# Kernel tuning notes

Hardware: AMD Instinct MI355X
Metric: run time of the kernel (lower is better)

Reference implementation:

```python
import math
import jax, jax.numpy as jnp
import numpy as np

H, D_H = 16, 128  # heads, head_dim; d = H*D_H = 2048

def _heads_view(w, rank):
    # w: (d, r) -> (H, r, d_h), matching torch view(H, d_h, r).transpose(1, 2)
    return jnp.transpose(w.reshape(H, D_H, rank), (0, 2, 1))

def setup_inputs() -> dict:
    key = jax.random.key(0)
    ks = jax.random.split(key, 9)
    d, rq, rk, rv = 2048, 512, 512, 512
    B, T = 2, 2048
    s = 0.02  # GPT-2 style init scale keeps logits numerically sane
    return {
        "x": jax.random.normal(ks[0], (B, T, d), dtype=jnp.float32),
        "q_down_w": jax.random.normal(ks[1], (rq, d), dtype=jnp.float32) * s,
        "k_down_w": jax.random.normal(ks[2], (rk, d), dtype=jnp.float32) * s,
        "v_down_w": jax.random.normal(ks[3], (rv, d), dtype=jnp.float32) * s,
        "q_up_w": jax.random.normal(ks[4], (d, rq), dtype=jnp.float32) * s,
        "k_up_w": jax.random.normal(ks[5], (d, rk), dtype=jnp.float32) * s,
        "v_up_w": jax.random.normal(ks[6], (d, rv), dtype=jnp.float32) * s,
        "out_w": jax.random.normal(ks[7], (d, d), dtype=jnp.float32) * s,
        "out_b": jnp.zeros((d,), dtype=jnp.float32),
    }

def reference(x, q_down_w, k_down_w, v_down_w, q_up_w, k_up_w, v_up_w, out_w, out_b):
    B, T, d = x.shape
    rq, rk, rv = q_down_w.shape[0], k_down_w.shape[0], v_down_w.shape[0]
    # Down projections (nn.Linear: x @ W^T)
    Qd = x @ q_down_w.T            # [B, T, rq]
    Kd = x @ k_down_w.T            # [B, S, rk] (S == T, no past_kv)
    Vd = x @ v_down_w.T            # [B, S, rv]
    S = Kd.shape[1]
    # Absorbed score matrix M: [H, rq, rk]
    Uq_h = _heads_view(q_up_w, rq)  # [H, rq, d_h]
    Uk_h = _heads_view(k_up_w, rk)  # [H, rk, d_h]
    M = jnp.einsum('hqd,hkd->hqk', Uq_h, Uk_h) * (1.0 / math.sqrt(D_H))
    # Logits via factorized path: [B,H,T,rk] then [B,H,T,S]
    Qm = jnp.einsum('btq,hqk->bhtk', Qd, M)
    logits = jnp.einsum('bhtk,bsk->bhts', Qm, Kd)
    # Causal mask (P = S - T = 0)
    P = S - T
    i = jnp.arange(T)[:, None]
    j = jnp.arange(S)[None, :]
    future = j > (P + i)
    logits = jnp.where(future[None, None], -jnp.inf, logits)
    attn = jax.nn.softmax(logits.astype(jnp.float32), axis=-1)
    attn = jnp.nan_to_num(attn).astype(x.dtype)
    # Values path
    Uv_h = _heads_view(v_up_w, rv)                      # [H, rv, d_h]
    V_up = jnp.einsum('bsr,hrd->bhsd', Vd, Uv_h)        # [B, H, S, d_h]
    ctx = jnp.einsum('bhts,bhsd->bhtd', attn, V_up)     # [B, H, T, d_h]
    ctx = jnp.transpose(ctx, (0, 2, 1, 3)).reshape(B, T, d)
    out = ctx @ out_w.T + out_b
    return out
```

## Files before the change

kernel.cpp:

```cpp
#include <hip/hip_runtime.h>
#include <stdint.h>

typedef __bf16 bf16x8 __attribute__((ext_vector_type(8)));
typedef float  f32x4  __attribute__((ext_vector_type(4)));
typedef float  f32x16 __attribute__((ext_vector_type(16)));
typedef unsigned short u16;
typedef unsigned int u32;
typedef u16 u16x8 __attribute__((ext_vector_type(8)));
typedef u32 u32x4 __attribute__((ext_vector_type(4)));

__device__ __forceinline__ u16 f2bf(float f) {
  uint32_t u = __builtin_bit_cast(uint32_t, f);
  u += 0x7fffu + ((u >> 16) & 1u);
  return (u16)(u >> 16);
}
__device__ __forceinline__ u32 cvtpk(float lo, float hi) {
  u32 r;
  asm("v_cvt_pk_bf16_f32 %0, %1, %2" : "=v"(r) : "v"(lo), "v"(hi));
  return r;
}

__device__ __forceinline__ void async_cp16(const void* src, void* lds) {
  __builtin_amdgcn_global_load_lds(
      (const __attribute__((address_space(1))) uint32_t*)src,
      (__attribute__((address_space(3))) uint32_t*)lds, 16, 0, 0);
}

struct CvtArgs {
  const float* in[8];
  u16* out[8];
  int n8[8];
  int nblk[8];
};
__global__ void cvt_multi(CvtArgs a) {
  int bx = blockIdx.x;
  int t = 0;
  while (t < 7 && bx >= a.nblk[t]) { bx -= a.nblk[t]; ++t; }
  const int i = bx * 256 + threadIdx.x;
  if (i >= a.n8[t]) return;
  const float4* p = (const float4*)a.in[t] + (size_t)i * 2;
  float4 va = p[0], vb = p[1];
  u16x8 r;
  r[0] = f2bf(va.x); r[1] = f2bf(va.y); r[2] = f2bf(va.z); r[3] = f2bf(va.w);
  r[4] = f2bf(vb.x); r[5] = f2bf(vb.y); r[6] = f2bf(vb.z); r[7] = f2bf(vb.w);
  ((u16x8*)a.out[t])[i] = r;
}

struct GemmB3 {
  const u16* A[3];
  const u16* Bm[3];
  u16* C[3];
  float alpha[3];
};

template<bool F32OUT>
__global__ __launch_bounds__(256, 2)
void gemm_bt(GemmB3 args, float* __restrict__ Cf, const float* __restrict__ bias,
             int M, int N, int K)
{
  __shared__ u16 At[128 * 64];
  __shared__ u16 Bt[128 * 64];
  const int z = blockIdx.z;
  const u16* __restrict__ A  = args.A[z];
  const u16* __restrict__ Bw = args.Bm[z];
  const int bm = blockIdx.x * 128;
  const int bn = blockIdx.y * 128;
  const int tid = threadIdx.x;
  const int w  = tid >> 6;
  const int l  = tid & 63;
  const int lr = l & 15;
  const int lg = l >> 4;
  const int wr = (w >> 1) * 64;
  const int wc = (w & 1) * 64;

  f32x4 acc[4][4];
  #pragma unroll
  for (int m = 0; m < 4; ++m)
    #pragma unroll
    for (int n = 0; n < 4; ++n) acc[m][n] = (f32x4){0.f, 0.f, 0.f, 0.f};

  for (int k0 = 0; k0 < K; k0 += 64) {
    __syncthreads();
    #pragma unroll
    for (int i = 0; i < 4; ++i) {
      const int slot = i * 256 + tid;
      const int row  = slot >> 3;
      const int pos  = slot & 7;
      const int gs   = pos ^ (row & 7);
      async_cp16(A  + (size_t)(bm + row) * K + k0 + gs * 8,
                 At + (size_t)(i * 256 + w * 64) * 8);
      async_cp16(Bw + (size_t)(bn + row) * K + k0 + gs * 8,
                 Bt + (size_t)(i * 256 + w * 64) * 8);
    }
    __syncthreads();
    #pragma unroll
    for (int kk = 0; kk < 2; ++kk) {
      bf16x8 af[4], bfr[4];
      #pragma unroll
      for (int m = 0; m < 4; ++m) {
        const int row = wr + m * 16 + lr;
        const int pos = (kk * 4 + lg) ^ (row & 7);
        af[m] = *(const bf16x8*)(At + row * 64 + pos * 8);
      }
      #pragma unroll
      for (int n = 0; n < 4; ++n) {
        const int row = wc + n * 16 + lr;
        const int pos = (kk * 4 + lg) ^ (row & 7);
        bfr[n] = *(const bf16x8*)(Bt + row * 64 + pos * 8);
      }
      #pragma unroll
      for (int m = 0; m < 4; ++m)
        #pragma unroll
        for (int n = 0; n < 4; ++n)
          acc[m][n] = __builtin_amdgcn_mfma_f32_16x16x32_bf16(af[m], bfr[n], acc[m][n], 0, 0, 0);
    }
  }

  if constexpr (F32OUT) {
    #pragma unroll
    for (int n = 0; n < 4; ++n) {
      const int col = bn + wc + n * 16 + lr;
      const float bv = bias[col];
      #pragma unroll
      for (int m = 0; m < 4; ++m) {
        const int rbase = bm + wr + m * 16 + lg * 4;
        #pragma unroll
        for (int j = 0; j < 4; ++j)
          Cf[(size_t)(rbase + j) * N + col] = acc[m][n][j] + bv;
      }
    }
  } else {
    u16* __restrict__ C = args.C[z];
    const float alpha = args.alpha[z];
    #pragma unroll
    for (int n = 0; n < 4; ++n) {
      const int col = bn + wc + n * 16 + lr;
      #pragma unroll
      for (int m = 0; m < 4; ++m) {
        const int rbase = bm + wr + m * 16 + lg * 4;
        #pragma unroll
        for (int j = 0; j < 4; ++j)
          C[(size_t)(rbase + j) * N + col] = f2bf(acc[m][n][j] * alpha);
      }
    }
  }
}

__global__ __launch_bounds__(256, 2)
void mla_attn(const u16* __restrict__ Qu, const u16* __restrict__ Ku,
              const u16* __restrict__ Vtg, u16* __restrict__ ctx)
{
  __shared__ u16 Ktb[2][64 * 128];
  __shared__ u16 Vtb[2][128 * 64];

  const int bid = blockIdx.x;
  const int kk  = bid >> 5;
  const int qt  = (kk < 8) ? kk : 23 - kk;
  const int bh  = bid & 31;
  const int b = bh >> 4, h = bh & 15;
  const int qbase = qt * 128;
  const int tid = threadIdx.x;
  const int w = tid >> 6, l = tid & 63;
  const int ql = l & 31;
  const int hi = l >> 5;
  const bool hb = (hi != 0);
  const int T = 2048;
  const size_t rs = 2048;

  const u16* Qp = Qu + ((size_t)b * T) * rs + (size_t)h * 128;
  const u16* Kp = Ku + ((size_t)b * T) * rs + (size_t)h * 128;
  const u16* Vp = Vtg + (size_t)(h * 128) * 4096 + (size_t)b * T;

  const int qw = qbase + w * 32;
  const int qg = qw + ql;

  bf16x8 qf[8];
  #pragma unroll
  for (int kb = 0; kb < 8; ++kb)
    qf[kb] = *(const bf16x8*)(Qp + (size_t)qg * rs + kb * 16 + hi * 8);

  f32x16 acc[4];
  #pragma unroll
  for (int dt = 0; dt < 4; ++dt)
    #pragma unroll
    for (int r = 0; r < 16; ++r) acc[dt][r] = 0.f;
  float mrun = -1.0e30f, lsum = 0.f;

  const int ksr = tid >> 4;
  const u16* kb0 = Kp + (size_t)ksr * rs + (((tid & 15) ^ (ksr & 15)) * 8);
  const int vsr = tid >> 3;
  const u16* vb0 = Vp + (size_t)vsr * 4096 + (((tid & 7) ^ (vsr & 7)) * 8);

  const int nT = 2 * qt + 2;

  auto stage = [&](int buf, int it) {
    const int s0 = it * 64;
    #pragma unroll
    for (int i = 0; i < 4; ++i)
      async_cp16(kb0 + (size_t)(s0 + i * 16) * rs, &Ktb[buf][(i * 256 + w * 64) * 8]);
    #pragma unroll
    for (int i = 0; i < 4; ++i)
      async_cp16(vb0 + (size_t)(i * 32) * 4096 + s0, &Vtb[buf][(i * 256 + w * 64) * 8]);
  };

  stage(0, 0);
  int cur = 0;

  for (int it = 0; it < nT; ++it) {
    __syncthreads();
    if (it + 1 < nT) stage(cur ^ 1, it + 1);
    const int s0 = it * 64;
    if (s0 <= qw + 31) {
      const u16* Kt = Ktb[cur];
      const u16* Vt = Vtb[cur];
      const bool diag = (it == (qw >> 6));

      f32x16 c0, c1;
      #pragma unroll
      for (int r = 0; r < 16; ++r) { c0[r] = 0.f; c1[r] = 0.f; }
      __builtin_amdgcn_s_setprio(1);
      #pragma unroll
      for (int kb = 0; kb < 8; ++kb) {
        bf16x8 kf0 = *(const bf16x8*)(Kt + ql * 128 + (((2 * kb + hi) ^ (ql & 15)) * 8));
        c0 = __builtin_amdgcn_mfma_f32_32x32x16_bf16(kf0, qf[kb], c0, 0, 0, 0);
      }
      #pragma unroll
      for (int kb = 0; kb < 8; ++kb) {
        bf16x8 kf1 = *(const bf16x8*)(Kt + (32 + ql) * 128 + (((2 * kb + hi) ^ (ql & 15)) * 8));
        c1 = __builtin_amdgcn_mfma_f32_32x32x16_bf16(kf1, qf[kb], c1, 0, 0, 0);
      }
      __builtin_amdgcn_s_setprio(0);

      float p[32];
      if (diag) {
        #pragma unroll
        for (int r = 0; r < 16; ++r) {
          const int sg0 = s0 + 4 * hi + (r & 3) + 8 * (r >> 2);
          p[r]      = (sg0      <= qg) ? c0[r] : -INFINITY;
          p[16 + r] = (sg0 + 32 <= qg) ? c1[r] : -INFINITY;
        }
      } else {
        #pragma unroll
        for (int r = 0; r < 16; ++r) { p[r] = c0[r]; p[16 + r] = c1[r]; }
      }
      float t16[16];
      #pragma unroll
      for (int r = 0; r < 16; ++r) t16[r] = fmaxf(p[r], p[16 + r]);
      float t8[8];
      #pragma unroll
      for (int r = 0; r < 8; ++r) t8[r] = fmaxf(t16[r], t16[8 + r]);
      float t4[4];
      #pragma unroll
      for (int r = 0; r < 4; ++r) t4[r] = fmaxf(t8[r], t8[4 + r]);
      float mx = fmaxf(fmaxf(t4[0], t4[1]), fmaxf(t4[2], t4[3]));
      mx = fmaxf(mx, __shfl_xor(mx, 32));
      if (__any(mx > mrun + 8.f)) {
        const float mnew = fmaxf(mrun, mx);
        const float scl = exp2f(mrun - mnew);
        mrun = mnew;
        lsum *= scl;
        #pragma unroll
        for (int dt = 0; dt < 4; ++dt)
          #pragma unroll
          for (int r = 0; r < 16; ++r) acc[dt][r] *= scl;
      }
      #pragma unroll
      for (int r = 0; r < 32; ++r) p[r] = exp2f(p[r] - mrun);
      float s16[16];
      #pragma unroll
      for (int r = 0; r < 16; ++r) s16[r] = p[r] + p[16 + r];
      float s8[8];
      #pragma unroll
      for (int r = 0; r < 8; ++r) s8[r] = s16[r] + s16[8 + r];
      float s4[4];
      #pragma unroll
      for (int r = 0; r < 4; ++r) s4[r] = s8[r] + s8[4 + r];
      float psum = (s4[0] + s4[1]) + (s4[2] + s4[3]);
      lsum += psum + __shfl_xor(psum, 32);

      bf16x8 fr[4];
      #pragma unroll
      for (int st = 0; st < 2; ++st) {
        const int o = st * 16;
        u32 P0 = cvtpk(p[o + 0], p[o + 1]),   P1 = cvtpk(p[o + 2], p[o + 3]);
        u32 P2 = cvtpk(p[o + 4], p[o + 5]),   P3 = cvtpk(p[o + 6], p[o + 7]);
        u32 P4 = cvtpk(p[o + 8], p[o + 9]),   P5 = cvtpk(p[o + 10], p[o + 11]);
        u32 P6 = cvtpk(p[o + 12], p[o + 13]), P7 = cvtpk(p[o + 14], p[o + 15]);
        u32 Y0 = __shfl_xor(hb ? P0 : P2, 32);
        u32 Y1 = __shfl_xor(hb ? P1 : P3, 32);
        u32 Y2 = __shfl_xor(hb ? P4 : P6, 32);
        u32 Y3 = __shfl_xor(hb ? P5 : P7, 32);
        fr[st * 2 + 0] = __builtin_bit_cast(bf16x8,
            (u32x4){hb ? Y0 : P0, hb ? Y1 : P1, hb ? P2 : Y0, hb ? P3 : Y1});
        fr[st * 2 + 1] = __builtin_bit_cast(bf16x8,
            (u32x4){hb ? Y2 : P4, hb ? Y3 : P5, hb ? P6 : Y2, hb ? P7 : Y3});
      }

      __builtin_amdgcn_s_setprio(1);
      #pragma unroll
      for (int dt = 0; dt < 4; ++dt) {
        const int vrow = (dt * 32 + ql) * 64;
        #pragma unroll
        for (int ks = 0; ks < 4; ++ks) {
          bf16x8 v = *(const bf16x8*)(Vt + vrow + (((2 * ks + hi) ^ (ql & 7)) * 8));
          acc[dt] = __builtin_amdgcn_mfma_f32_32x32x16_bf16(v, fr[ks], acc[dt], 0, 0, 0);
        }
      }
      __builtin_amdgcn_s_setprio(0);
    }
    cur ^= 1;
  }

  __syncthreads();
  u16* Ot = &Ktb[0][0];
  const float inv = 1.f / lsum;
  const int orow = w * 32 + ql;
  #pragma unroll
  for (int dt = 0; dt < 4; ++dt) {
    #pragma unroll
    for (int rq = 0; rq < 4; ++rq) {
      const int dhb = dt * 32 + 8 * rq + 4 * hi;
      const int dhs = dhb ^ ((ql & 15) << 3);
      u16 e0 = f2bf(acc[dt][rq * 4 + 0] * inv);
      u16 e1 = f2bf(acc[dt][rq * 4 + 1] * inv);
      u16 e2 = f2bf(acc[dt][rq * 4 + 2] * inv);
      u16 e3 = f2bf(acc[dt][rq * 4 + 3] * inv);
      u32 w0 = (u32)e0 | ((u32)e1 << 16);
      u32 w1 = (u32)e2 | ((u32)e3 << 16);
      *(u32*)(Ot + orow * 128 + dhs)     = w0;
      *(u32*)(Ot + orow * 128 + dhs + 2) = w1;
    }
  }
  __syncthreads();
  #pragma unroll
  for (int i = 0; i < 8; ++i) {
    const int n = i * 256 + tid;
    const int q = n >> 4, g = n & 15;
    bf16x8 v = *(const bf16x8*)(Ot + q * 128 + ((g ^ (q & 15)) * 8));
    *(bf16x8*)(ctx + ((size_t)b * T + qbase + q) * rs + h * 128 + g * 8) = v;
  }
}

extern "C" void kernel_launch(void* const* d_in, const int* in_sizes, int n_in,
                              void* d_out, int out_size, void* d_ws, size_t ws_size,
                              hipStream_t stream)
{
  (void)n_in; (void)out_size; (void)ws_size;
  const float* x   = (const float*)d_in[0];
  const float* qdw = (const float*)d_in[1];
  const float* kdw = (const float*)d_in[2];
  const float* vdw = (const float*)d_in[3];
  const float* quw = (const float*)d_in[4];
  const float* kuw = (const float*)d_in[5];
  const float* vuw = (const float*)d_in[6];
  const float* oww = (const float*)d_in[7];
  const float* ob  = (const float*)d_in[8];

  const int d = 2048, r = 512;
  const int BT = in_sizes[0] / d;

  u16* p = (u16*)d_ws;
  auto take = [&](size_t n) { u16* q = p; p += n; return q; };
  u16* xb  = take((size_t)BT * d);
  u16* wqd = take((size_t)r * d);
  u16* wkd = take((size_t)r * d);
  u16* wvd = take((size_t)r * d);
  u16* wqu = take((size_t)d * r);
  u16* wku = take((size_t)d * r);
  u16* wvu = take((size_t)d * r);
  u16* wow = take((size_t)d * d);
  u16* Qd  = take((size_t)BT * r);
  u16* Kd  = take((size_t)BT * r);
  u16* Vd  = take((size_t)BT * r);
  u16* Qu  = take((size_t)BT * d);
  u16* Ku  = take((size_t)BT * d);
  u16* Vtg = take((size_t)BT * d);
  u16* ctx = take((size_t)BT * d);

  CvtArgs ca;
  const float* ins[8] = {x, oww, qdw, kdw, vdw, quw, kuw, vuw};
  u16* outs[8]        = {xb, wow, wqd, wkd, wvd, wqu, wku, wvu};
  const size_t ns[8]  = {(size_t)BT * d, (size_t)d * d,
                         (size_t)r * d, (size_t)r * d, (size_t)r * d,
                         (size_t)d * r, (size_t)d * r, (size_t)d * r};
  int total_blk = 0;
  for (int t = 0; t < 8; ++t) {
    ca.in[t] = ins[t]; ca.out[t] = outs[t];
    ca.n8[t] = (int)(ns[t] / 8);
    ca.nblk[t] = (ca.n8[t] + 255) / 256;
    total_blk += ca.nblk[t];
  }
  cvt_multi<<<dim3(total_blk), dim3(256), 0, stream>>>(ca);

  GemmB3 g1;
  g1.A[0] = xb;  g1.A[1] = xb;  g1.A[2] = xb;
  g1.Bm[0] = wqd; g1.Bm[1] = wkd; g1.Bm[2] = wvd;
  g1.C[0] = Qd;  g1.C[1] = Kd;  g1.C[2] = Vd;
  g1.alpha[0] = 1.f; g1.alpha[1] = 1.f; g1.alpha[2] = 1.f;
  gemm_bt<false><<<dim3(BT / 128, r / 128, 3), dim3(256), 0, stream>>>(
      g1, nullptr, nullptr, BT, r, d);

  GemmB3 g2;
  g2.A[0] = Qd;  g2.A[1] = Kd;  g2.A[2] = Kd;
  g2.Bm[0] = wqu; g2.Bm[1] = wku; g2.Bm[2] = wku;
  g2.C[0] = Qu;  g2.C[1] = Ku;  g2.C[2] = Ku;
  g2.alpha[0] = 0.12751743f; g2.alpha[1] = 1.f; g2.alpha[2] = 1.f;
  gemm_bt<false><<<dim3(BT / 128, d / 128, 2), dim3(256), 0, stream>>>(
      g2, nullptr, nullptr, BT, d, r);

  GemmB3 g2v;
  g2v.A[0] = wvu; g2v.A[1] = wvu; g2v.A[2] = wvu;
  g2v.Bm[0] = Vd; g2v.Bm[1] = Vd; g2v.Bm[2] = Vd;
  g2v.C[0] = Vtg; g2v.C[1] = Vtg; g2v.C[2] = Vtg;
  g2v.alpha[0] = 1.f; g2v.alpha[1] = 1.f; g2v.alpha[2] = 1.f;
  gemm_bt<false><<<dim3(d / 128, BT / 128, 1), dim3(256), 0, stream>>>(
      g2v, nullptr, nullptr, d, BT, r);

  mla_attn<<<dim3(512), dim3(256), 0, stream>>>(Qu, Ku, Vtg, ctx);

  GemmB3 g3;
  g3.A[0] = ctx; g3.A[1] = ctx; g3.A[2] = ctx;
  g3.Bm[0] = wow; g3.Bm[1] = wow; g3.Bm[2] = wow;
  g3.C[0] = nullptr; g3.C[1] = nullptr; g3.C[2] = nullptr;
  g3.alpha[0] = 1.f; g3.alpha[1] = 1.f; g3.alpha[2] = 1.f;
  gemm_bt<true><<<dim3(BT / 128, d / 128, 1), dim3(256), 0, stream>>>(
      g3, (float*)d_out, ob, BT, d, d);
}
```

Before: 225.4 us.

## Use single-wave attention blocks loading K/V directly from global memory

Restructures the attention kernel from 256-thread blocks sharing 128 query rows, with double-buffered LDS staging of K/V tiles, to 64-thread single-wave blocks that each own 32 query rows. K and V fragments are read straight from global memory into registers, longest-first. This removes LDS staging, barriers and the idle waves on causal tails, and gives finer load balancing across 2048 blocks. The cost is that K/V tiles are no longer shared across four waves, so global/L2 traffic rises and memory latency is no longer hidden by async prefetch.

Result: slower. 381.4 us (+69.2%).

```diff
diff --git a/kernel.cpp b/kernel.cpp
--- a/kernel.cpp
+++ b/kernel.cpp
@@ -146,21 +146,18 @@
   }
 }
 
-__global__ __launch_bounds__(256, 2)
+__global__ __launch_bounds__(64, 4)
 void mla_attn(const u16* __restrict__ Qu, const u16* __restrict__ Ku,
               const u16* __restrict__ Vtg, u16* __restrict__ ctx)
 {
-  __shared__ u16 Ktb[2][64 * 128];
-  __shared__ u16 Vtb[2][128 * 64];
+  __shared__ u16 Ot[32 * 128];
 
   const int bid = blockIdx.x;
-  const int kk  = bid >> 5;
-  const int qt  = (kk < 8) ? kk : 23 - kk;
+  const int qi  = bid >> 5;
   const int bh  = bid & 31;
   const int b = bh >> 4, h = bh & 15;
-  const int qbase = qt * 128;
-  const int tid = threadIdx.x;
-  const int w = tid >> 6, l = tid & 63;
+  const int qw = (63 - qi) * 32;
+  const int l = threadIdx.x & 63;
   const int ql = l & 31;
   const int hi = l >> 5;
   const bool hb = (hi != 0);
@@ -171,7 +168,6 @@
   const u16* Kp = Ku + ((size_t)b * T) * rs + (size_t)h * 128;
   const u16* Vp = Vtg + (size_t)(h * 128) * 4096 + (size_t)b * T;
 
-  const int qw = qbase + w * 32;
   const int qg = qw + ql;
 
   bf16x8 qf[8];
@@ -179,6 +175,9 @@
   for (int kb = 0; kb < 8; ++kb)
     qf[kb] = *(const bf16x8*)(Qp + (size_t)qg * rs + kb * 16 + hi * 8);
 
+  const u16* kA = Kp + (size_t)ql * rs + hi * 8;
+  const u16* vA = Vp + (size_t)ql * 4096 + hi * 8;
+
   f32x16 acc[4];
   #pragma unroll
   for (int dt = 0; dt < 4; ++dt)
@@ -186,135 +185,107 @@
     for (int r = 0; r < 16; ++r) acc[dt][r] = 0.f;
   float mrun = -1.0e30f, lsum = 0.f;
 
-  const int ksr = tid >> 4;
-  const u16* kb0 = Kp + (size_t)ksr * rs + (((tid & 15) ^ (ksr & 15)) * 8);
-  const int vsr = tid >> 3;
-  const u16* vb0 = Vp + (size_t)vsr * 4096 + (((tid & 7) ^ (vsr & 7)) * 8);
-
-  const int nT = 2 * qt + 2;
-
-  auto stage = [&](int buf, int it) {
+  const int nIt = (qw >> 6) + 1;
+
+  for (int it = 0; it < nIt; ++it) {
     const int s0 = it * 64;
-    #pragma unroll
-    for (int i = 0; i < 4; ++i)
-      async_cp16(kb0 + (size_t)(s0 + i * 16) * rs, &Ktb[buf][(i * 256 + w * 64) * 8]);
-    #pragma unroll
-    for (int i = 0; i < 4; ++i)
-      async_cp16(vb0 + (size_t)(i * 32) * 4096 + s0, &Vtb[buf][(i * 256 + w * 64) * 8]);
-  };
-
-  stage(0, 0);
-  int cur = 0;
-
-  for (int it = 0; it < nT; ++it) {
-    __syncthreads();
-    if (it + 1 < nT) stage(cur ^ 1, it + 1);
-    const int s0 = it * 64;
-    if (s0 <= qw + 31) {
-      const u16* Kt = Ktb[cur];
-      const u16* Vt = Vtb[cur];
-      const bool diag = (it == (qw >> 6));
-
-      f32x16 c0, c1;
-      #pragma unroll
-      for (int r = 0; r < 16; ++r) { c0[r] = 0.f; c1[r] = 0.f; }
-      __builtin_amdgcn_s_setprio(1);
-      #pragma unroll
-      for (int kb = 0; kb < 8; ++kb) {
-        bf16x8 kf0 = *(const bf16x8*)(Kt + ql * 128 + (((2 * kb + hi) ^ (ql & 15)) * 8));
-        c0 = __builtin_amdgcn_mfma_f32_32x32x16_bf16(kf0, qf[kb], c0, 0, 0, 0);
-      }
-      #pragma unroll
-      for (int kb = 0; kb < 8; ++kb) {
-        bf16x8 kf1 = *(const bf16x8*)(Kt + (32 + ql) * 128 + (((2 * kb + hi) ^ (ql & 15)) * 8));
-        c1 = __builtin_amdgcn_mfma_f32_32x32x16_bf16(kf1, qf[kb], c1, 0, 0, 0);
-      }
-      __builtin_amdgcn_s_setprio(0);
-
-      float p[32];
-      if (diag) {
+    const bool diag = (it == nIt - 1);
+
+    f32x16 c0, c1;
+    #pragma unroll
+    for (int r = 0; r < 16; ++r) { c0[r] = 0.f; c1[r] = 0.f; }
+    __builtin_amdgcn_s_setprio(1);
+    #pragma unroll
+    for (int kb = 0; kb < 8; ++kb) {
+      bf16x8 kf0 = *(const bf16x8*)(kA + (size_t)s0 * rs + kb * 16);
+      c0 = __builtin_amdgcn_mfma_f32_32x32x16_bf16(kf0, qf[kb], c0, 0, 0, 0);
+    }
+    #pragma unroll
+    for (int kb = 0; kb < 8; ++kb) {
+      bf16x8 kf1 = *(const bf16x8*)(kA + (size_t)(s0 + 32) * rs + kb * 16);
+      c1 = __builtin_amdgcn_mfma_f32_32x32x16_bf16(kf1, qf[kb], c1, 0, 0, 0);
+    }
+    __builtin_amdgcn_s_setprio(0);
+
+    float p[32];
+    if (diag) {
+      #pragma unroll
+      for (int r = 0; r < 16; ++r) {
+        const int sg0 = s0 + 4 * hi + (r & 3) + 8 * (r >> 2);
+        p[r]      = (sg0      <= qg) ? c0[r] : -INFINITY;
+        p[16 + r] = (sg0 + 32 <= qg) ? c1[r] : -INFINITY;
+      }
+    } else {
+      #pragma unroll
+      for (int r = 0; r < 16; ++r) { p[r] = c0[r]; p[16 + r] = c1[r]; }
+    }
+    float t16[16];
+    #pragma unroll
+    for (int r = 0; r < 16; ++r) t16[r] = fmaxf(p[r], p[16 + r]);
+    float t8[8];
+    #pragma unroll
+    for (int r = 0; r < 8; ++r) t8[r] = fmaxf(t16[r], t16[8 + r]);
+    float t4[4];
+    #pragma unroll
+    for (int r = 0; r < 4; ++r) t4[r] = fmaxf(t8[r], t8[4 + r]);
+    float mx = fmaxf(fmaxf(t4[0], t4[1]), fmaxf(t4[2], t4[3]));
+    mx = fmaxf(mx, __shfl_xor(mx, 32));
+    if (__any(mx > mrun + 8.f)) {
+      const float mnew = fmaxf(mrun, mx);
+      const float scl = exp2f(mrun - mnew);
+      mrun = mnew;
+      lsum *= scl;
+      #pragma unroll
+      for (int dt = 0; dt < 4; ++dt)
         #pragma unroll
-        for (int r = 0; r < 16; ++r) {
-          const int sg0 = s0 + 4 * hi + (r & 3) + 8 * (r >> 2);
-          p[r]      = (sg0      <= qg) ? c0[r] : -INFINITY;
-          p[16 + r] = (sg0 + 32 <= qg) ? c1[r] : -INFINITY;
-        }
-      } else {
-        #pragma unroll
-        for (int r = 0; r < 16; ++r) { p[r] = c0[r]; p[16 + r] = c1[r]; }
-      }
-      float t16[16];
-      #pragma unroll
-      for (int r = 0; r < 16; ++r) t16[r] = fmaxf(p[r], p[16 + r]);
-      float t8[8];
-      #pragma unroll
-      for (int r = 0; r < 8; ++r) t8[r] = fmaxf(t16[r], t16[8 + r]);
-      float t4[4];
-      #pragma unroll
-      for (int r = 0; r < 4; ++r) t4[r] = fmaxf(t8[r], t8[4 + r]);
-      float mx = fmaxf(fmaxf(t4[0], t4[1]), fmaxf(t4[2], t4[3]));
-      mx = fmaxf(mx, __shfl_xor(mx, 32));
-      if (__any(mx > mrun + 8.f)) {
-        const float mnew = fmaxf(mrun, mx);
-        const float scl = exp2f(mrun - mnew);
-        mrun = mnew;
-        lsum *= scl;
-        #pragma unroll
-        for (int dt = 0; dt < 4; ++dt)
-          #pragma unroll
-          for (int r = 0; r < 16; ++r) acc[dt][r] *= scl;
-      }
-      #pragma unroll
-      for (int r = 0; r < 32; ++r) p[r] = exp2f(p[r] - mrun);
-      float s16[16];
-      #pragma unroll
-      for (int r = 0; r < 16; ++r) s16[r] = p[r] + p[16 + r];
-      float s8[8];
-      #pragma unroll
-      for (int r = 0; r < 8; ++r) s8[r] = s16[r] + s16[8 + r];
-      float s4[4];
-      #pragma unroll
-      for (int r = 0; r < 4; ++r) s4[r] = s8[r] + s8[4 + r];
-      float psum = (s4[0] + s4[1]) + (s4[2] + s4[3]);
-      lsum += psum + __shfl_xor(psum, 32);
-
-      bf16x8 fr[4];
-      #pragma unroll
-      for (int st = 0; st < 2; ++st) {
-        const int o = st * 16;
-        u32 P0 = cvtpk(p[o + 0], p[o + 1]),   P1 = cvtpk(p[o + 2], p[o + 3]);
-        u32 P2 = cvtpk(p[o + 4], p[o + 5]),   P3 = cvtpk(p[o + 6], p[o + 7]);
-        u32 P4 = cvtpk(p[o + 8], p[o + 9]),   P5 = cvtpk(p[o + 10], p[o + 11]);
-        u32 P6 = cvtpk(p[o + 12], p[o + 13]), P7 = cvtpk(p[o + 14], p[o + 15]);
-        u32 Y0 = __shfl_xor(hb ? P0 : P2, 32);
-        u32 Y1 = __shfl_xor(hb ? P1 : P3, 32);
-        u32 Y2 = __shfl_xor(hb ? P4 : P6, 32);
-        u32 Y3 = __shfl_xor(hb ? P5 : P7, 32);
-        fr[st * 2 + 0] = __builtin_bit_cast(bf16x8,
-            (u32x4){hb ? Y0 : P0, hb ? Y1 : P1, hb ? P2 : Y0, hb ? P3 : Y1});
-        fr[st * 2 + 1] = __builtin_bit_cast(bf16x8,
-            (u32x4){hb ? Y2 : P4, hb ? Y3 : P5, hb ? P6 : Y2, hb ? P7 : Y3});
-      }
-
-      __builtin_amdgcn_s_setprio(1);
-      #pragma unroll
-      for (int dt = 0; dt < 4; ++dt) {
-        const int vrow = (dt * 32 + ql) * 64;
-        #pragma unroll
-        for (int ks = 0; ks < 4; ++ks) {
-          bf16x8 v = *(const bf16x8*)(Vt + vrow + (((2 * ks + hi) ^ (ql & 7)) * 8));
-          acc[dt] = __builtin_amdgcn_mfma_f32_32x32x16_bf16(v, fr[ks], acc[dt], 0, 0, 0);
-        }
-      }
-      __builtin_amdgcn_s_setprio(0);
-    }
-    cur ^= 1;
-  }
-
-  __syncthreads();
-  u16* Ot = &Ktb[0][0];
+        for (int r = 0; r < 16; ++r) acc[dt][r] *= scl;
+    }
+    #pragma unroll
+    for (int r = 0; r < 32; ++r) p[r] = exp2f(p[r] - mrun);
+    float s16[16];
+    #pragma unroll
+    for (int r = 0; r < 16; ++r) s16[r] = p[r] + p[16 + r];
+    float s8[8];
+    #pragma unroll
+    for (int r = 0; r < 8; ++r) s8[r] = s16[r] + s16[8 + r];
+    float s4[4];
+    #pragma unroll
+    for (int r = 0; r < 4; ++r) s4[r] = s8[r] + s8[4 + r];
+    float psum = (s4[0] + s4[1]) + (s4[2] + s4[3]);
+    lsum += psum + __shfl_xor(psum, 32);
+
+    bf16x8 fr[4];
+    #pragma unroll
+    for (int st = 0; st < 2; ++st) {
+      const int o = st * 16;
+      u32 P0 = cvtpk(p[o + 0], p[o + 1]),   P1 = cvtpk(p[o + 2], p[o + 3]);
+      u32 P2 = cvtpk(p[o + 4], p[o + 5]),   P3 = cvtpk(p[o + 6], p[o + 7]);
+      u32 P4 = cvtpk(p[o + 8], p[o + 9]),   P5 = cvtpk(p[o + 10], p[o + 11]);
+      u32 P6 = cvtpk(p[o + 12], p[o + 13]), P7 = cvtpk(p[o + 14], p[o + 15]);
+      u32 Y0 = __shfl_xor(hb ? P0 : P2, 32);
+      u32 Y1 = __shfl_xor(hb ? P1 : P3, 32);
+      u32 Y2 = __shfl_xor(hb ? P4 : P6, 32);
+      u32 Y3 = __shfl_xor(hb ? P5 : P7, 32);
+      fr[st * 2 + 0] = __builtin_bit_cast(bf16x8,
+          (u32x4){hb ? Y0 : P0, hb ? Y1 : P1, hb ? P2 : Y0, hb ? P3 : Y1});
+      fr[st * 2 + 1] = __builtin_bit_cast(bf16x8,
+          (u32x4){hb ? Y2 : P4, hb ? Y3 : P5, hb ? P6 : Y2, hb ? P7 : Y3});
+    }
+
+    __builtin_amdgcn_s_setprio(1);
+    #pragma unroll
+    for (int dt = 0; dt < 4; ++dt) {
+      const u16* vrow = vA + (size_t)(dt * 32) * 4096 + s0;
+      #pragma unroll
+      for (int ks = 0; ks < 4; ++ks) {
+        bf16x8 v = *(const bf16x8*)(vrow + ks * 16);
+        acc[dt] = __builtin_amdgcn_mfma_f32_32x32x16_bf16(v, fr[ks], acc[dt], 0, 0, 0);
+      }
+    }
+    __builtin_amdgcn_s_setprio(0);
+  }
+
   const float inv = 1.f / lsum;
-  const int orow = w * 32 + ql;
   #pragma unroll
   for (int dt = 0; dt < 4; ++dt) {
     #pragma unroll
@@ -327,17 +298,17 @@
       u16 e3 = f2bf(acc[dt][rq * 4 + 3] * inv);
       u32 w0 = (u32)e0 | ((u32)e1 << 16);
       u32 w1 = (u32)e2 | ((u32)e3 << 16);
-      *(u32*)(Ot + orow * 128 + dhs)     = w0;
-      *(u32*)(Ot + orow * 128 + dhs + 2) = w1;
+      *(u32*)(Ot + ql * 128 + dhs)     = w0;
+      *(u32*)(Ot + ql * 128 + dhs + 2) = w1;
     }
   }
   __syncthreads();
   #pragma unroll
   for (int i = 0; i < 8; ++i) {
-    const int n = i * 256 + tid;
+    const int n = i * 64 + l;
     const int q = n >> 4, g = n & 15;
     bf16x8 v = *(const bf16x8*)(Ot + q * 128 + ((g ^ (q & 15)) * 8));
-    *(bf16x8*)(ctx + ((size_t)b * T + qbase + q) * rs + h * 128 + g * 8) = v;
+    *(bf16x8*)(ctx + ((size_t)b * T + qw + q) * rs + h * 128 + g * 8) = v;
   }
 }
 
@@ -416,7 +387,7 @@
   gemm_bt<false><<<dim3(d / 128, BT / 128, 1), dim3(256), 0, stream>>>(
       g2v, nullptr, nullptr, d, BT, r);
 
-  mla_attn<<<dim3(512), dim3(256), 0, stream>>>(Qu, Ku, Vtg, ctx);
+  mla_attn<<<dim3(2048), dim3(64), 0, stream>>>(Qu, Ku, Vtg, ctx);
 
   GemmB3 g3;
   g3.A[0] = ctx; g3.A[1] = ctx; g3.A[2] = ctx;
```

## Double-buffer GEMM LDS tiles and merge V up-projection into batched launch

Applied to the files above, without the earlier changes.

The bf16 GEMM kernel now keeps two LDS buffers, so the async global-to-LDS copy of the next K tile is issued before computing on the current one, with a single barrier per iteration. It also raises wave priority around the MFMA block. The separate V up-projection GEMM is folded into the Q/K up-projection launch as a third z-slice, using per-slice N and a block-index swap, which removes one launch and lets all three run concurrently. Doubling LDS use to 64KB per block may reduce occupancy relative to the two-blocks-per-CU launch bound.

After: 206.4 us. 1.09x faster.

```diff
diff --git a/kernel.cpp b/kernel.cpp
--- a/kernel.cpp
+++ b/kernel.cpp
@@ -51,20 +51,24 @@
   const u16* Bm[3];
   u16* C[3];
   float alpha[3];
+  int Nz[3];
 };
 
 template<bool F32OUT>
 __global__ __launch_bounds__(256, 2)
 void gemm_bt(GemmB3 args, float* __restrict__ Cf, const float* __restrict__ bias,
-             int M, int N, int K)
+             int K, int zswap)
 {
-  __shared__ u16 At[128 * 64];
-  __shared__ u16 Bt[128 * 64];
+  __shared__ u16 At[2][128 * 64];
+  __shared__ u16 Bt[2][128 * 64];
   const int z = blockIdx.z;
   const u16* __restrict__ A  = args.A[z];
   const u16* __restrict__ Bw = args.Bm[z];
-  const int bm = blockIdx.x * 128;
-  const int bn = blockIdx.y * 128;
+  const int N = args.Nz[z];
+  int bx = blockIdx.x, by = blockIdx.y;
+  if (z == zswap) { const int t = bx; bx = by; by = t; }
+  const int bm = bx * 128;
+  const int bn = by * 128;
   const int tid = threadIdx.x;
   const int w  = tid >> 6;
   const int l  = tid & 63;
@@ -79,8 +83,7 @@
     #pragma unroll
     for (int n = 0; n < 4; ++n) acc[m][n] = (f32x4){0.f, 0.f, 0.f, 0.f};
 
-  for (int k0 = 0; k0 < K; k0 += 64) {
-    __syncthreads();
+  auto stage = [&](int buf, int k0) {
     #pragma unroll
     for (int i = 0; i < 4; ++i) {
       const int slot = i * 256 + tid;
@@ -88,11 +91,19 @@
       const int pos  = slot & 7;
       const int gs   = pos ^ (row & 7);
       async_cp16(A  + (size_t)(bm + row) * K + k0 + gs * 8,
-                 At + (size_t)(i * 256 + w * 64) * 8);
+                 &At[buf][(i * 256 + w * 64) * 8]);
       async_cp16(Bw + (size_t)(bn + row) * K + k0 + gs * 8,
-                 Bt + (size_t)(i * 256 + w * 64) * 8);
-    }
+                 &Bt[buf][(i * 256 + w * 64) * 8]);
+    }
+  };
+
+  const int nk = K >> 6;
+  stage(0, 0);
+  int cur = 0;
+
+  for (int t = 0; t < nk; ++t) {
     __syncthreads();
+    if (t + 1 < nk) stage(cur ^ 1, (t + 1) * 64);
     #pragma unroll
     for (int kk = 0; kk < 2; ++kk) {
       bf16x8 af[4], bfr[4];
@@ -100,20 +111,23 @@
       for (int m = 0; m < 4; ++m) {
         const int row = wr + m * 16 + lr;
         const int pos = (kk * 4 + lg) ^ (row & 7);
-        af[m] = *(const bf16x8*)(At + row * 64 + pos * 8);
+        af[m] = *(const bf16x8*)(&At[cur][row * 64 + pos * 8]);
       }
       #pragma unroll
       for (int n = 0; n < 4; ++n) {
         const int row = wc + n * 16 + lr;
         const int pos = (kk * 4 + lg) ^ (row & 7);
-        bfr[n] = *(const bf16x8*)(Bt + row * 64 + pos * 8);
-      }
+        bfr[n] = *(const bf16x8*)(&Bt[cur][row * 64 + pos * 8]);
+      }
+      __builtin_amdgcn_s_setprio(1);
       #pragma unroll
       for (int m = 0; m < 4; ++m)
         #pragma unroll
         for (int n = 0; n < 4; ++n)
           acc[m][n] = __builtin_amdgcn_mfma_f32_16x16x32_bf16(af[m], bfr[n], acc[m][n], 0, 0, 0);
-    }
+      __builtin_amdgcn_s_setprio(0);
+    }
+    cur ^= 1;
   }
 
   if constexpr (F32OUT) {
@@ -397,24 +411,18 @@
   g1.Bm[0] = wqd; g1.Bm[1] = wkd; g1.Bm[2] = wvd;
   g1.C[0] = Qd;  g1.C[1] = Kd;  g1.C[2] = Vd;
   g1.alpha[0] = 1.f; g1.alpha[1] = 1.f; g1.alpha[2] = 1.f;
+  g1.Nz[0] = r; g1.Nz[1] = r; g1.Nz[2] = r;
   gemm_bt<false><<<dim3(BT / 128, r / 128, 3), dim3(256), 0, stream>>>(
-      g1, nullptr, nullptr, BT, r, d);
+      g1, nullptr, nullptr, d, -1);
 
   GemmB3 g2;
-  g2.A[0] = Qd;  g2.A[1] = Kd;  g2.A[2] = Kd;
-  g2.Bm[0] = wqu; g2.Bm[1] = wku; g2.Bm[2] = wku;
-  g2.C[0] = Qu;  g2.C[1] = Ku;  g2.C[2] = Ku;
+  g2.A[0] = Qd;  g2.A[1] = Kd;  g2.A[2] = wvu;
+  g2.Bm[0] = wqu; g2.Bm[1] = wku; g2.Bm[2] = Vd;
+  g2.C[0] = Qu;  g2.C[1] = Ku;  g2.C[2] = Vtg;
   g2.alpha[0] = 0.12751743f; g2.alpha[1] = 1.f; g2.alpha[2] = 1.f;
-  gemm_bt<false><<<dim3(BT / 128, d / 128, 2), dim3(256), 0, stream>>>(
-      g2, nullptr, nullptr, BT, d, r);
-
-  GemmB3 g2v;
-  g2v.A[0] = wvu; g2v.A[1] = wvu; g2v.A[2] = wvu;
-  g2v.Bm[0] = Vd; g2v.Bm[1] = Vd; g2v.Bm[2] = Vd;
-  g2v.C[0] = Vtg; g2v.C[1] = Vtg; g2v.C[2] = Vtg;
-  g2v.alpha[0] = 1.f; g2v.alpha[1] = 1.f; g2v.alpha[2] = 1.f;
-  gemm_bt<false><<<dim3(d / 128, BT / 128, 1), dim3(256), 0, stream>>>(
-      g2v, nullptr, nullptr, d, BT, r);
+  g2.Nz[0] = d; g2.Nz[1] = d; g2.Nz[2] = BT;
+  gemm_bt<false><<<dim3(BT / 128, d / 128, 3), dim3(256), 0, stream>>>(
+      g2, nullptr, nullptr, r, 2);
 
   mla_attn<<<dim3(512), dim3(256), 0, stream>>>(Qu, Ku, Vtg, ctx);
 
@@ -423,6 +431,7 @@
   g3.Bm[0] = wow; g3.Bm[1] = wow; g3.Bm[2] = wow;
   g3.C[0] = nullptr; g3.C[1] = nullptr; g3.C[2] = nullptr;
   g3.alpha[0] = 1.f; g3.alpha[1] = 1.f; g3.alpha[2] = 1.f;
+  g3.Nz[0] = d; g3.Nz[1] = d; g3.Nz[2] = d;
   gemm_bt<true><<<dim3(BT / 128, d / 128, 1), dim3(256), 0, stream>>>(
-      g3, (float*)d_out, ob, BT, d, d);
-}
+      g3, (float*)d_out, ob, d, -1);
+}
```
